# Optimization experiments

Hardware: AMD Instinct MI355X
Metric: run time of the kernel (lower is better)

Reference implementation:

```python
import jax, jax.numpy as jnp
import numpy as np

N, F, F_, H = 8192, 1024, 64, 4
LEAKY_ALPHA = 0.2
MASK_VAL = -1e10


def setup_inputs() -> dict:
    key = jax.random.key(0)
    k1, k2, k3, k4 = jax.random.split(key, 4)
    X = jax.random.normal(k1, (N, F), dtype=jnp.float32)
    # sparse-ish binary adjacency with self loops (A = A + I in the source script)
    A = (jax.random.uniform(k2, (N, N)) < 0.004).astype(jnp.float32)
    A = jnp.clip(A + jnp.eye(N, dtype=jnp.float32), 0.0, 1.0)
    W = jax.random.normal(k3, (H, F, F_), dtype=jnp.float32) * (1.0 / np.sqrt(F))
    attn_a = jax.random.normal(k4, (H, 2 * F_, 1), dtype=jnp.float32) * (1.0 / np.sqrt(2 * F_))
    bias = jnp.zeros((H, F_), dtype=jnp.float32)
    return {"X": X, "A": A, "W": W, "attn_a": attn_a, "bias": bias}


def reference(X, A, W, attn_a, bias):
    # features per head: [H, N, F_]
    feats = jnp.einsum('nf,hfk->hnk', X, W)
    # concat-score trick: [f_i, f_j] @ a == f_i @ a[:F_] + f_j @ a[F_:]
    a_self = attn_a[:, :F_, 0]   # [H, F_]
    a_neigh = attn_a[:, F_:, 0]  # [H, F_]
    s_self = jnp.einsum('hnk,hk->hn', feats, a_self)   # [H, N]
    s_neigh = jnp.einsum('hnk,hk->hn', feats, a_neigh)  # [H, N]
    scores = s_self[:, :, None] + s_neigh[:, None, :]   # [H, N, N]
    scores = jnp.where(scores > 0, scores, LEAKY_ALPHA * scores)  # LeakyReLU(0.2)
    scores = scores + MASK_VAL * (1.0 - A)[None]
    attn = jax.nn.softmax(scores, axis=-1)              # [H, N, N]
    # aggregate (dropout is identity at inference)
    out = jnp.einsum('hij,hjk->hik', attn, feats) + bias[:, None, :]  # [H, N, F_]
    out = jnp.transpose(out, (1, 0, 2)).reshape(X.shape[0], H * F_)   # concat heads
    return jax.nn.relu(out)
```

## Files before the change

### kernel.cpp

```cpp
#include <hip/hip_runtime.h>
#include <hip/hip_bf16.h>
#include <stdint.h>

#define NN 8192
#define FF 1024
#define FD 64
#define NH 4
#define CC 256
#define MAXE 192

typedef __attribute__((ext_vector_type(8))) short short8;
typedef __attribute__((ext_vector_type(4))) short short4v;
typedef __attribute__((ext_vector_type(4))) float f32x4;

__device__ __forceinline__ short bf16_rne(float f) {
    union { float f; uint32_t u; } v; v.f = f;
    uint32_t r = (v.u + 0x7FFFu + ((v.u >> 16) & 1u)) >> 16;
    return (short)(r & 0xFFFFu);
}
__device__ __forceinline__ float bf2f(short s) {
    union { uint32_t u; float f; } v; v.u = ((uint32_t)(uint16_t)s) << 16;
    return v.f;
}

__global__ __launch_bounds__(256) void scan_kernel(const float* __restrict__ A,
                                                   int* __restrict__ nbr,
                                                   int* __restrict__ cnt) {
    __shared__ int idx[MAXE];
    __shared__ int c;
    const int row = blockIdx.x;
    const int t = threadIdx.x;
    if (t == 0) c = 0;
    __syncthreads();
    const f32x4* A4 = (const f32x4*)(A + (size_t)row * NN);
    for (int r = 0; r < 8; ++r) {
        int c4 = r * 256 + t;
        f32x4 v = __builtin_nontemporal_load(&A4[c4]);
        if (v.x > 0.5f) { int p = atomicAdd(&c, 1); if (p < MAXE) idx[p] = c4 * 4 + 0; }
        if (v.y > 0.5f) { int p = atomicAdd(&c, 1); if (p < MAXE) idx[p] = c4 * 4 + 1; }
        if (v.z > 0.5f) { int p = atomicAdd(&c, 1); if (p < MAXE) idx[p] = c4 * 4 + 2; }
        if (v.w > 0.5f) { int p = atomicAdd(&c, 1); if (p < MAXE) idx[p] = c4 * 4 + 3; }
    }
    __syncthreads();
    int n = min(c, MAXE);
    if (t < n) nbr[row * MAXE + t] = idx[t];
    if (t == 0) cnt[row] = n;
}

__global__ __launch_bounds__(256) void wt_kernel(const float* __restrict__ W,
                                                 short* __restrict__ Wt) {
    int gid = blockIdx.x * 256 + threadIdx.x;
    int k = gid & 1023;
    int n = (gid >> 10) & 63;
    int h = gid >> 16;
    Wt[gid] = bf16_rne(W[(h << 16) + k * 64 + n]);
}

__global__ __launch_bounds__(256) void xb_kernel(const float* __restrict__ X,
                                                 short* __restrict__ Xb) {
    int gid = blockIdx.x * 256 + threadIdx.x;
    float4 v = ((const float4*)X)[gid];
    short4 o;
    o.x = bf16_rne(v.x); o.y = bf16_rne(v.y);
    o.z = bf16_rne(v.z); o.w = bf16_rne(v.w);
    ((short4*)Xb)[gid] = o;
}

__global__ __launch_bounds__(256) void gemm_kernel(const short* __restrict__ Xb,
                                                   const short* __restrict__ Wt,
                                                   const float* __restrict__ attn_a,
                                                   short* __restrict__ featb,
                                                   float* __restrict__ s_self,
                                                   float* __restrict__ s_neigh) {
    __shared__ short Xs[64 * 40];
    __shared__ short Ws[64 * 40];
    const int h  = blockIdx.x;
    const int m0 = blockIdx.y * 64;
    const int t  = threadIdx.x;
    const int wave = t >> 6, lane = t & 63;
    const int q = lane >> 4, nl = lane & 15;
    const int srow = t >> 2, sk8 = (t & 3) * 8;

    f32x4 acc0 = {0.f,0.f,0.f,0.f}, acc1 = {0.f,0.f,0.f,0.f};
    f32x4 acc2 = {0.f,0.f,0.f,0.f}, acc3 = {0.f,0.f,0.f,0.f};

    const short* Xp = Xb + (size_t)(m0 + srow) * FF + sk8;
    const short* Wp = Wt + (size_t)(h * 64 + srow) * FF + sk8;

    for (int k0 = 0; k0 < FF; k0 += 32) {
        short8 xv = *(const short8*)(Xp + k0);
        short8 wv = *(const short8*)(Wp + k0);
        *(short8*)(&Xs[srow * 40 + sk8]) = xv;
        *(short8*)(&Ws[srow * 40 + sk8]) = wv;
        __syncthreads();
        short8 a  = *(const short8*)(&Xs[(wave * 16 + nl) * 40 + q * 8]);
        short8 b0 = *(const short8*)(&Ws[( 0 + nl) * 40 + q * 8]);
        short8 b1 = *(const short8*)(&Ws[(16 + nl) * 40 + q * 8]);
        short8 b2 = *(const short8*)(&Ws[(32 + nl) * 40 + q * 8]);
        short8 b3 = *(const short8*)(&Ws[(48 + nl) * 40 + q * 8]);
        acc0 = __builtin_amdgcn_mfma_f32_16x16x32_bf16(a, b0, acc0, 0, 0, 0);
        acc1 = __builtin_amdgcn_mfma_f32_16x16x32_bf16(a, b1, acc1, 0, 0, 0);
        acc2 = __builtin_amdgcn_mfma_f32_16x16x32_bf16(a, b2, acc2, 0, 0, 0);
        acc3 = __builtin_amdgcn_mfma_f32_16x16x32_bf16(a, b3, acc3, 0, 0, 0);
        __syncthreads();
    }
    const int row = m0 + wave * 16 + q * 4;
    const int colbase = h * 64 + nl;
    for (int r = 0; r < 4; ++r) {
        short* fr = featb + (size_t)(row + r) * CC + colbase;
        fr[ 0] = bf16_rne(acc0[r]);
        fr[16] = bf16_rne(acc1[r]);
        fr[32] = bf16_rne(acc2[r]);
        fr[48] = bf16_rne(acc3[r]);
    }
    const float A0 = attn_a[h * 128 + nl],      A1 = attn_a[h * 128 + nl + 16];
    const float A2 = attn_a[h * 128 + nl + 32], A3 = attn_a[h * 128 + nl + 48];
    const float B0 = attn_a[h * 128 + 64 + nl],      B1 = attn_a[h * 128 + 64 + nl + 16];
    const float B2 = attn_a[h * 128 + 64 + nl + 32], B3 = attn_a[h * 128 + 64 + nl + 48];
    for (int r = 0; r < 4; ++r) {
        float ps = acc0[r] * A0 + acc1[r] * A1 + acc2[r] * A2 + acc3[r] * A3;
        float pn = acc0[r] * B0 + acc1[r] * B1 + acc2[r] * B2 + acc3[r] * B3;
        for (int off = 1; off < 16; off <<= 1) {
            ps += __shfl_xor(ps, off);
            pn += __shfl_xor(pn, off);
        }
        if (nl == 0) {
            s_self [h * NN + row + r] = ps;
            s_neigh[h * NN + row + r] = pn;
        }
    }
}

__global__ __launch_bounds__(256) void smax_kernel(const int* __restrict__ nbr,
                                                   const int* __restrict__ cnt,
                                                   const short* __restrict__ featb,
                                                   const float* __restrict__ s_self,
                                                   const float* __restrict__ s_neigh,
                                                   const float* __restrict__ bias,
                                                   float* __restrict__ out) {
    __shared__ int js[MAXE];
    __shared__ float ps[NH][MAXE];
    const int row = blockIdx.x;
    const int t = threadIdx.x;
    const int h = t >> 6, lane = t & 63;
    const int n = cnt[row];
    if (t < n) js[t] = nbr[row * MAXE + t];
    __syncthreads();

    const float si = s_self[h * NN + row];
    const float* snh = s_neigh + h * NN;

    float sc[3];
    #pragma unroll
    for (int i = 0; i < 3; ++i) {
        int e = lane + 64 * i;
        float s = -1e30f;
        if (e < n) {
            s = si + snh[js[e]];
            s = s > 0.f ? s : 0.2f * s;
        }
        sc[i] = s;
    }
    float m = fmaxf(sc[0], fmaxf(sc[1], sc[2]));
    for (int off = 1; off < 64; off <<= 1) m = fmaxf(m, __shfl_xor(m, off));

    float dsum = 0.f;
    #pragma unroll
    for (int i = 0; i < 3; ++i) {
        int e = lane + 64 * i;
        if (e < n) {
            float p = __expf(sc[i] - m);
            ps[h][e] = p;
            dsum += p;
        }
    }
    for (int off = 1; off < 64; off <<= 1) dsum += __shfl_xor(dsum, off);

    const int sub = lane >> 4;
    const int l16 = lane & 15;
    const short* fb = featb + h * 64 + l16 * 4;
    f32x4 acc = {0.f, 0.f, 0.f, 0.f};
    #pragma unroll 2
    for (int e = sub; e < n; e += 4) {
        int j = js[e];
        float p = ps[h][e];
        short4v f = *(const short4v*)(fb + (size_t)j * CC);
        acc[0] = fmaf(p, bf2f(f.x), acc[0]);
        acc[1] = fmaf(p, bf2f(f.y), acc[1]);
        acc[2] = fmaf(p, bf2f(f.z), acc[2]);
        acc[3] = fmaf(p, bf2f(f.w), acc[3]);
    }
    #pragma unroll
    for (int k = 0; k < 4; ++k) {
        acc[k] += __shfl_xor(acc[k], 16);
        acc[k] += __shfl_xor(acc[k], 32);
    }
    if (sub == 0) {
        float rd = 1.0f / dsum;
        f32x4 o;
        #pragma unroll
        for (int k = 0; k < 4; ++k)
            o[k] = fmaxf(acc[k] * rd + bias[h * 64 + l16 * 4 + k], 0.f);
        *(f32x4*)(out + (size_t)row * CC + h * 64 + l16 * 4) = o;
    }
}

extern "C" void kernel_launch(void* const* d_in, const int* in_sizes, int n_in,
                              void* d_out, int out_size, void* d_ws, size_t ws_size,
                              hipStream_t stream) {
    const float* X      = (const float*)d_in[0];
    const float* A      = (const float*)d_in[1];
    const float* W      = (const float*)d_in[2];
    const float* attn_a = (const float*)d_in[3];
    const float* bias   = (const float*)d_in[4];
    float* out = (float*)d_out;

    char* ws = (char*)d_ws;
    short* featb   = (short*)ws;
    float* s_self  = (float*)(ws + 4194304);
    float* s_neigh = (float*)(ws + 4325376);
    short* Wt      = (short*)(ws + 4456448);
    short* Xb      = (short*)(ws + 4980736);
    int*   nbr     = (int*)  (ws + 21757952);
    int*   cnt     = (int*)  (ws + 28049408);

    scan_kernel<<<NN, 256, 0, stream>>>(A, nbr, cnt);
    wt_kernel  <<<1024, 256, 0, stream>>>(W, Wt);
    xb_kernel  <<<8192, 256, 0, stream>>>(X, Xb);
    gemm_kernel<<<dim3(4, 128), 256, 0, stream>>>(Xb, Wt, attn_a, featb, s_self, s_neigh);
    smax_kernel<<<NN, 256, 0, stream>>>(nbr, cnt, featb, s_self, s_neigh, bias, out);
}
```

Before: 404.0 us.

## Fuse X conversion into GEMM and co-schedule adjacency scan in one kernel

Removes the separate X-to-bf16 kernel by converting fp32 X on the fly inside the GEMM tile loads. It also merges the adjacency scan and the GEMM into one launch using block-index partitioning, so the bandwidth-bound scan can overlap the compute-bound GEMM. Attention scores move to a row-major [N,4] layout so one vector load fetches all heads per neighbor, and the aggregation loop uses 16-byte loads with 8 neighbor groups. The trade-off is that the GEMM now reads twice the X bytes per tile, plus extra conversion work and register pressure in the mixed kernel.

Result: no change. 406.6 us (+0.6%).

```diff
diff --git a/kernel.cpp b/kernel.cpp
--- a/kernel.cpp
+++ b/kernel.cpp
@@ -10,7 +10,6 @@
 #define MAXE 192
 
 typedef __attribute__((ext_vector_type(8))) short short8;
-typedef __attribute__((ext_vector_type(4))) short short4v;
 typedef __attribute__((ext_vector_type(4))) float f32x4;
 
 __device__ __forceinline__ short bf16_rne(float f) {
@@ -21,30 +20,6 @@
 __device__ __forceinline__ float bf2f(short s) {
     union { uint32_t u; float f; } v; v.u = ((uint32_t)(uint16_t)s) << 16;
     return v.f;
-}
-
-__global__ __launch_bounds__(256) void scan_kernel(const float* __restrict__ A,
-                                                   int* __restrict__ nbr,
-                                                   int* __restrict__ cnt) {
-    __shared__ int idx[MAXE];
-    __shared__ int c;
-    const int row = blockIdx.x;
-    const int t = threadIdx.x;
-    if (t == 0) c = 0;
-    __syncthreads();
-    const f32x4* A4 = (const f32x4*)(A + (size_t)row * NN);
-    for (int r = 0; r < 8; ++r) {
-        int c4 = r * 256 + t;
-        f32x4 v = __builtin_nontemporal_load(&A4[c4]);
-        if (v.x > 0.5f) { int p = atomicAdd(&c, 1); if (p < MAXE) idx[p] = c4 * 4 + 0; }
-        if (v.y > 0.5f) { int p = atomicAdd(&c, 1); if (p < MAXE) idx[p] = c4 * 4 + 1; }
-        if (v.z > 0.5f) { int p = atomicAdd(&c, 1); if (p < MAXE) idx[p] = c4 * 4 + 2; }
-        if (v.w > 0.5f) { int p = atomicAdd(&c, 1); if (p < MAXE) idx[p] = c4 * 4 + 3; }
-    }
-    __syncthreads();
-    int n = min(c, MAXE);
-    if (t < n) nbr[row * MAXE + t] = idx[t];
-    if (t == 0) cnt[row] = n;
 }
 
 __global__ __launch_bounds__(256) void wt_kernel(const float* __restrict__ W,
@@ -56,90 +31,112 @@
     Wt[gid] = bf16_rne(W[(h << 16) + k * 64 + n]);
 }
 
-__global__ __launch_bounds__(256) void xb_kernel(const float* __restrict__ X,
-                                                 short* __restrict__ Xb) {
-    int gid = blockIdx.x * 256 + threadIdx.x;
-    float4 v = ((const float4*)X)[gid];
-    short4 o;
-    o.x = bf16_rne(v.x); o.y = bf16_rne(v.y);
-    o.z = bf16_rne(v.z); o.w = bf16_rne(v.w);
-    ((short4*)Xb)[gid] = o;
-}
-
-__global__ __launch_bounds__(256) void gemm_kernel(const short* __restrict__ Xb,
+__global__ __launch_bounds__(256) void mega_kernel(const float* __restrict__ X,
                                                    const short* __restrict__ Wt,
                                                    const float* __restrict__ attn_a,
+                                                   const float* __restrict__ A,
                                                    short* __restrict__ featb,
-                                                   float* __restrict__ s_self,
-                                                   float* __restrict__ s_neigh) {
+                                                   float* __restrict__ s_self4,
+                                                   float* __restrict__ s_neigh4,
+                                                   int* __restrict__ nbr,
+                                                   int* __restrict__ cnt) {
     __shared__ short Xs[64 * 40];
     __shared__ short Ws[64 * 40];
-    const int h  = blockIdx.x;
-    const int m0 = blockIdx.y * 64;
-    const int t  = threadIdx.x;
-    const int wave = t >> 6, lane = t & 63;
-    const int q = lane >> 4, nl = lane & 15;
-    const int srow = t >> 2, sk8 = (t & 3) * 8;
-
-    f32x4 acc0 = {0.f,0.f,0.f,0.f}, acc1 = {0.f,0.f,0.f,0.f};
-    f32x4 acc2 = {0.f,0.f,0.f,0.f}, acc3 = {0.f,0.f,0.f,0.f};
-
-    const short* Xp = Xb + (size_t)(m0 + srow) * FF + sk8;
-    const short* Wp = Wt + (size_t)(h * 64 + srow) * FF + sk8;
-
-    for (int k0 = 0; k0 < FF; k0 += 32) {
-        short8 xv = *(const short8*)(Xp + k0);
-        short8 wv = *(const short8*)(Wp + k0);
-        *(short8*)(&Xs[srow * 40 + sk8]) = xv;
-        *(short8*)(&Ws[srow * 40 + sk8]) = wv;
+    const int b = blockIdx.x;
+    const int t = threadIdx.x;
+
+    if (b < 512) {
+        const int h  = b & 3;
+        const int m0 = (b >> 2) * 64;
+        const int wave = t >> 6, lane = t & 63;
+        const int q = lane >> 4, nl = lane & 15;
+        const int srow = t >> 2, sk8 = (t & 3) * 8;
+
+        f32x4 acc0 = {0.f,0.f,0.f,0.f}, acc1 = {0.f,0.f,0.f,0.f};
+        f32x4 acc2 = {0.f,0.f,0.f,0.f}, acc3 = {0.f,0.f,0.f,0.f};
+
+        const float* Xp = X + (size_t)(m0 + srow) * FF + sk8;
+        const short* Wp = Wt + (size_t)(h * 64 + srow) * FF + sk8;
+
+        for (int k0 = 0; k0 < FF; k0 += 32) {
+            float4 x0 = *(const float4*)(Xp + k0);
+            float4 x1 = *(const float4*)(Xp + k0 + 4);
+            short8 wv = *(const short8*)(Wp + k0);
+            short8 xv;
+            xv[0] = bf16_rne(x0.x); xv[1] = bf16_rne(x0.y);
+            xv[2] = bf16_rne(x0.z); xv[3] = bf16_rne(x0.w);
+            xv[4] = bf16_rne(x1.x); xv[5] = bf16_rne(x1.y);
+            xv[6] = bf16_rne(x1.z); xv[7] = bf16_rne(x1.w);
+            *(short8*)(&Xs[srow * 40 + sk8]) = xv;
+            *(short8*)(&Ws[srow * 40 + sk8]) = wv;
+            __syncthreads();
+            short8 a  = *(const short8*)(&Xs[(wave * 16 + nl) * 40 + q * 8]);
+            short8 b0 = *(const short8*)(&Ws[( 0 + nl) * 40 + q * 8]);
+            short8 b1 = *(const short8*)(&Ws[(16 + nl) * 40 + q * 8]);
+            short8 b2 = *(const short8*)(&Ws[(32 + nl) * 40 + q * 8]);
+            short8 b3 = *(const short8*)(&Ws[(48 + nl) * 40 + q * 8]);
+            acc0 = __builtin_amdgcn_mfma_f32_16x16x32_bf16(a, b0, acc0, 0, 0, 0);
+            acc1 = __builtin_amdgcn_mfma_f32_16x16x32_bf16(a, b1, acc1, 0, 0, 0);
+            acc2 = __builtin_amdgcn_mfma_f32_16x16x32_bf16(a, b2, acc2, 0, 0, 0);
+            acc3 = __builtin_amdgcn_mfma_f32_16x16x32_bf16(a, b3, acc3, 0, 0, 0);
+            __syncthreads();
+        }
+        const int row = m0 + wave * 16 + q * 4;
+        const int colbase = h * 64 + nl;
+        for (int r = 0; r < 4; ++r) {
+            short* fr = featb + (size_t)(row + r) * CC + colbase;
+            fr[ 0] = bf16_rne(acc0[r]);
+            fr[16] = bf16_rne(acc1[r]);
+            fr[32] = bf16_rne(acc2[r]);
+            fr[48] = bf16_rne(acc3[r]);
+        }
+        const float A0 = attn_a[h * 128 + nl],      A1 = attn_a[h * 128 + nl + 16];
+        const float A2 = attn_a[h * 128 + nl + 32], A3 = attn_a[h * 128 + nl + 48];
+        const float B0 = attn_a[h * 128 + 64 + nl],      B1 = attn_a[h * 128 + 64 + nl + 16];
+        const float B2 = attn_a[h * 128 + 64 + nl + 32], B3 = attn_a[h * 128 + 64 + nl + 48];
+        for (int r = 0; r < 4; ++r) {
+            float ps = acc0[r] * A0 + acc1[r] * A1 + acc2[r] * A2 + acc3[r] * A3;
+            float pn = acc0[r] * B0 + acc1[r] * B1 + acc2[r] * B2 + acc3[r] * B3;
+            for (int off = 1; off < 16; off <<= 1) {
+                ps += __shfl_xor(ps, off);
+                pn += __shfl_xor(pn, off);
+            }
+            if (nl == 0) {
+                s_self4 [(row + r) * 4 + h] = ps;
+                s_neigh4[(row + r) * 4 + h] = pn;
+            }
+        }
+    } else {
+        int* idx = (int*)Xs;
+        int* c   = (int*)Ws;
+        const int row = b - 512;
+        if (t == 0) *c = 0;
         __syncthreads();
-        short8 a  = *(const short8*)(&Xs[(wave * 16 + nl) * 40 + q * 8]);
-        short8 b0 = *(const short8*)(&Ws[( 0 + nl) * 40 + q * 8]);
-        short8 b1 = *(const short8*)(&Ws[(16 + nl) * 40 + q * 8]);
-        short8 b2 = *(const short8*)(&Ws[(32 + nl) * 40 + q * 8]);
-        short8 b3 = *(const short8*)(&Ws[(48 + nl) * 40 + q * 8]);
-        acc0 = __builtin_amdgcn_mfma_f32_16x16x32_bf16(a, b0, acc0, 0, 0, 0);
-        acc1 = __builtin_amdgcn_mfma_f32_16x16x32_bf16(a, b1, acc1, 0, 0, 0);
-        acc2 = __builtin_amdgcn_mfma_f32_16x16x32_bf16(a, b2, acc2, 0, 0, 0);
-        acc3 = __builtin_amdgcn_mfma_f32_16x16x32_bf16(a, b3, acc3, 0, 0, 0);
+        const f32x4* A4 = (const f32x4*)(A + (size_t)row * NN);
+        for (int r = 0; r < 8; ++r) {
+            int c4 = r * 256 + t;
+            f32x4 v = __builtin_nontemporal_load(&A4[c4]);
+            if (v.x > 0.5f) { int p = atomicAdd(c, 1); if (p < MAXE) idx[p] = c4 * 4 + 0; }
+            if (v.y > 0.5f) { int p = atomicAdd(c, 1); if (p < MAXE) idx[p] = c4 * 4 + 1; }
+            if (v.z > 0.5f) { int p = atomicAdd(c, 1); if (p < MAXE) idx[p] = c4 * 4 + 2; }
+            if (v.w > 0.5f) { int p = atomicAdd(c, 1); if (p < MAXE) idx[p] = c4 * 4 + 3; }
+        }
         __syncthreads();
-    }
-    const int row = m0 + wave * 16 + q * 4;
-    const int colbase = h * 64 + nl;
-    for (int r = 0; r < 4; ++r) {
-        short* fr = featb + (size_t)(row + r) * CC + colbase;
-        fr[ 0] = bf16_rne(acc0[r]);
-        fr[16] = bf16_rne(acc1[r]);
-        fr[32] = bf16_rne(acc2[r]);
-        fr[48] = bf16_rne(acc3[r]);
-    }
-    const float A0 = attn_a[h * 128 + nl],      A1 = attn_a[h * 128 + nl + 16];
-    const float A2 = attn_a[h * 128 + nl + 32], A3 = attn_a[h * 128 + nl + 48];
-    const float B0 = attn_a[h * 128 + 64 + nl],      B1 = attn_a[h * 128 + 64 + nl + 16];
-    const float B2 = attn_a[h * 128 + 64 + nl + 32], B3 = attn_a[h * 128 + 64 + nl + 48];
-    for (int r = 0; r < 4; ++r) {
-        float ps = acc0[r] * A0 + acc1[r] * A1 + acc2[r] * A2 + acc3[r] * A3;
-        float pn = acc0[r] * B0 + acc1[r] * B1 + acc2[r] * B2 + acc3[r] * B3;
-        for (int off = 1; off < 16; off <<= 1) {
-            ps += __shfl_xor(ps, off);
-            pn += __shfl_xor(pn, off);
-        }
-        if (nl == 0) {
-            s_self [h * NN + row + r] = ps;
-            s_neigh[h * NN + row + r] = pn;
-        }
+        int n = min(*c, MAXE);
+        if (t < n) nbr[row * MAXE + t] = idx[t];
+        if (t == 0) cnt[row] = n;
     }
 }
 
 __global__ __launch_bounds__(256) void smax_kernel(const int* __restrict__ nbr,
                                                    const int* __restrict__ cnt,
                                                    const short* __restrict__ featb,
-                                                   const float* __restrict__ s_self,
-                                                   const float* __restrict__ s_neigh,
+                                                   const float* __restrict__ s_self4,
+                                                   const float* __restrict__ s_neigh4,
                                                    const float* __restrict__ bias,
                                                    float* __restrict__ out) {
     __shared__ int js[MAXE];
-    __shared__ float ps[NH][MAXE];
+    __shared__ float scs[NH][MAXE];
     const int row = blockIdx.x;
     const int t = threadIdx.x;
     const int h = t >> 6, lane = t & 63;
@@ -147,61 +144,74 @@
     if (t < n) js[t] = nbr[row * MAXE + t];
     __syncthreads();
 
-    const float si = s_self[h * NN + row];
-    const float* snh = s_neigh + h * NN;
-
-    float sc[3];
+    const f32x4 ss = *(const f32x4*)(s_self4 + row * 4);
+    if (t < n) {
+        f32x4 sn = *(const f32x4*)(s_neigh4 + js[t] * 4);
+        #pragma unroll
+        for (int hh = 0; hh < NH; ++hh) {
+            float s = ss[hh] + sn[hh];
+            scs[hh][t] = s > 0.f ? s : 0.2f * s;
+        }
+    }
+    __syncthreads();
+
+    float m = -1e30f;
     #pragma unroll
     for (int i = 0; i < 3; ++i) {
         int e = lane + 64 * i;
-        float s = -1e30f;
-        if (e < n) {
-            s = si + snh[js[e]];
-            s = s > 0.f ? s : 0.2f * s;
-        }
-        sc[i] = s;
-    }
-    float m = fmaxf(sc[0], fmaxf(sc[1], sc[2]));
+        if (e < n) m = fmaxf(m, scs[h][e]);
+    }
     for (int off = 1; off < 64; off <<= 1) m = fmaxf(m, __shfl_xor(m, off));
-
     float dsum = 0.f;
     #pragma unroll
     for (int i = 0; i < 3; ++i) {
         int e = lane + 64 * i;
         if (e < n) {
-            float p = __expf(sc[i] - m);
-            ps[h][e] = p;
+            float p = __expf(scs[h][e] - m);
+            scs[h][e] = p;
             dsum += p;
         }
     }
     for (int off = 1; off < 64; off <<= 1) dsum += __shfl_xor(dsum, off);
 
-    const int sub = lane >> 4;
-    const int l16 = lane & 15;
-    const short* fb = featb + h * 64 + l16 * 4;
-    f32x4 acc = {0.f, 0.f, 0.f, 0.f};
-    #pragma unroll 2
-    for (int e = sub; e < n; e += 4) {
+    const int sub = lane >> 3;
+    const int l8  = lane & 7;
+    const short* fb = featb + h * 64 + l8 * 8;
+    f32x4 accA = {0.f,0.f,0.f,0.f}, accB = {0.f,0.f,0.f,0.f};
+    for (int e = sub; e < n; e += 8) {
         int j = js[e];
-        float p = ps[h][e];
-        short4v f = *(const short4v*)(fb + (size_t)j * CC);
-        acc[0] = fmaf(p, bf2f(f.x), acc[0]);
-        acc[1] = fmaf(p, bf2f(f.y), acc[1]);
-        acc[2] = fmaf(p, bf2f(f.z), acc[2]);
-        acc[3] = fmaf(p, bf2f(f.w), acc[3]);
+        float p = scs[h][e];
+        short8 f = *(const short8*)(fb + (size_t)j * CC);
+        accA[0] = fmaf(p, bf2f(f[0]), accA[0]);
+        accA[1] = fmaf(p, bf2f(f[1]), accA[1]);
+        accA[2] = fmaf(p, bf2f(f[2]), accA[2]);
+        accA[3] = fmaf(p, bf2f(f[3]), accA[3]);
+        accB[0] = fmaf(p, bf2f(f[4]), accB[0]);
+        accB[1] = fmaf(p, bf2f(f[5]), accB[1]);
+        accB[2] = fmaf(p, bf2f(f[6]), accB[2]);
+        accB[3] = fmaf(p, bf2f(f[7]), accB[3]);
     }
     #pragma unroll
     for (int k = 0; k < 4; ++k) {
-        acc[k] += __shfl_xor(acc[k], 16);
-        acc[k] += __shfl_xor(acc[k], 32);
+        accA[k] += __shfl_xor(accA[k], 8);
+        accA[k] += __shfl_xor(accA[k], 16);
+        accA[k] += __shfl_xor(accA[k], 32);
+        accB[k] += __shfl_xor(accB[k], 8);
+        accB[k] += __shfl_xor(accB[k], 16);
+        accB[k] += __shfl_xor(accB[k], 32);
     }
     if (sub == 0) {
         float rd = 1.0f / dsum;
-        f32x4 o;
+        const float* bp = bias + h * 64 + l8 * 8;
+        f32x4 oA, oB;
         #pragma unroll
-        for (int k = 0; k < 4; ++k)
-            o[k] = fmaxf(acc[k] * rd + bias[h * 64 + l16 * 4 + k], 0.f);
-        *(f32x4*)(out + (size_t)row * CC + h * 64 + l16 * 4) = o;
+        for (int k = 0; k < 4; ++k) {
+            oA[k] = fmaxf(accA[k] * rd + bp[k],     0.f);
+            oB[k] = fmaxf(accB[k] * rd + bp[k + 4], 0.f);
+        }
+        float* op = out + (size_t)row * CC + h * 64 + l8 * 8;
+        *(f32x4*)op       = oA;
+        *(f32x4*)(op + 4) = oB;
     }
 }
 
@@ -216,17 +226,15 @@
     float* out = (float*)d_out;
 
     char* ws = (char*)d_ws;
-    short* featb   = (short*)ws;
-    float* s_self  = (float*)(ws + 4194304);
-    float* s_neigh = (float*)(ws + 4325376);
-    short* Wt      = (short*)(ws + 4456448);
-    short* Xb      = (short*)(ws + 4980736);
-    int*   nbr     = (int*)  (ws + 21757952);
-    int*   cnt     = (int*)  (ws + 28049408);
-
-    scan_kernel<<<NN, 256, 0, stream>>>(A, nbr, cnt);
+    short* featb    = (short*)ws;
+    float* s_self4  = (float*)(ws + 4194304);
+    float* s_neigh4 = (float*)(ws + 4325376);
+    short* Wt       = (short*)(ws + 4456448);
+    int*   nbr      = (int*)  (ws + 4980736);
+    int*   cnt      = (int*)  (ws + 11272192);
+
     wt_kernel  <<<1024, 256, 0, stream>>>(W, Wt);
-    xb_kernel  <<<8192, 256, 0, stream>>>(X, Xb);
-    gemm_kernel<<<dim3(4, 128), 256, 0, stream>>>(Xb, Wt, attn_a, featb, s_self, s_neigh);
-    smax_kernel<<<NN, 256, 0, stream>>>(nbr, cnt, featb, s_self, s_neigh, bias, out);
-}
+    mega_kernel<<<512 + NN, 256, 0, stream>>>(X, Wt, attn_a, A,
+                                              featb, s_self4, s_neigh4, nbr, cnt);
+    smax_kernel<<<NN, 256, 0, stream>>>(nbr, cnt, featb, s_self4, s_neigh4, bias, out);
+}
```
